# Kernel optimization log

Measured on AMD Instinct MI355X. Metric: run time of the kernel, lower is better.

## Reference

```python
import jax, jax.numpy as jnp
import numpy as np

NUM_CORRESPONDENCES = 256
M, N, D = 8192, 8192, 256


def setup_inputs() -> dict:
    key = jax.random.key(0)
    k1, k2 = jax.random.split(key)
    ref = jax.random.normal(k1, (M, D), dtype=jnp.float32)
    src = jax.random.normal(k2, (N, D), dtype=jnp.float32)
    # pairwise_distance(normalized=True) assumes unit-norm features
    ref = ref / jnp.linalg.norm(ref, axis=-1, keepdims=True)
    src = src / jnp.linalg.norm(src, axis=-1, keepdims=True)
    return {"ref_feats": ref, "src_feats": src}


def reference(ref_feats, src_feats):
    # squared pairwise distance for normalized feats: ||r||^2 + ||s||^2 - 2 r.s = 2 - 2 r.s
    dist = 2.0 - 2.0 * jnp.einsum('md,nd->mn', ref_feats, src_feats)  # [M, N]
    scores = jnp.exp(-dist)
    # dual normalization: row-normalized * col-normalized
    ref_scores = scores / jnp.sum(scores, axis=1, keepdims=True)
    src_scores = scores / jnp.sum(scores, axis=0, keepdims=True)
    scores = ref_scores * src_scores
    n_cols = scores.shape[1]
    flat = scores.reshape(-1)
    k = min(NUM_CORRESPONDENCES, flat.shape[0])
    corr_scores, corr_indices = jax.lax.top_k(flat, k)
    ref_corr_indices = corr_indices // n_cols
    src_corr_indices = corr_indices % n_cols
    # masks are None -> ref_indices/src_indices are identity arange, no remap needed
    return ref_corr_indices, src_corr_indices, corr_scores
```

## Files before the change

kernel.cpp:

```cpp
#include <hip/hip_runtime.h>

#define MD 8192
#define ND 8192
#define DD 256
#define KTOP 256
#define CAND_T0 0.26f
#define NCAP 4096
#define NPAD 4096

typedef unsigned int u32;
typedef unsigned short u16;
typedef unsigned long long u64;

#define OFF_R    0
#define OFF_CP   65536
#define OFF_CNT  589824
#define OFF_CAND 589952
#define OFF_KEYS 606336
#define OFF_A16  655360
#define OFF_B16  (OFF_A16 + 4194304)
#define WS_REQ   (OFF_B16 + 4194304)

using f16x8 = __attribute__((ext_vector_type(8))) _Float16;
using f32x4  = __attribute__((ext_vector_type(4))) float;

#define AS1 __attribute__((address_space(1)))
#define AS3 __attribute__((address_space(3)))

__device__ __forceinline__ u16 f2h(float x) {
  union { _Float16 h; u16 u; } v;
  v.h = (_Float16)x;
  return v.u;
}

__global__ void k_init(double* __restrict__ R, double* __restrict__ CP, int* __restrict__ cnt) {
  int stride = gridDim.x * blockDim.x;
  for (int i = blockIdx.x * blockDim.x + threadIdx.x; i < MD + 8 * ND; i += stride) {
    if (i < MD) R[i] = 0.0;
    else CP[i - MD] = 0.0;
  }
  if (blockIdx.x == 0 && threadIdx.x == 0) *cnt = 0;
}

__global__ __launch_bounds__(256) void k_prep2(
    const float* __restrict__ A, const float* __restrict__ B,
    u16* __restrict__ A16p, u16* __restrict__ B16p,
    double* __restrict__ R, double* __restrict__ CP, int* __restrict__ cnt) {
  const int gid = blockIdx.x * 256 + threadIdx.x;
  if (gid < MD) R[gid] = 0.0;
  if (gid < 8 * ND) CP[gid] = 0.0;
  if (gid == 0) *cnt = 0;

  {
    float4 v = ((const float4*)A)[gid];
    ushort4 h;
    h.x = f2h(v.x); h.y = f2h(v.y); h.z = f2h(v.z); h.w = f2h(v.w);
    ((ushort4*)A16p)[gid] = h;
  }
  {
    float4 v = ((const float4*)B)[gid];
    ushort4 h;
    h.x = f2h(v.x); h.y = f2h(v.y); h.z = f2h(v.z); h.w = f2h(v.w);
    ((ushort4*)B16p)[gid] = h;
  }
}

__global__ __launch_bounds__(512, 2) void k_gemm_mfma(
    const u16* __restrict__ A16, const u16* __restrict__ B16,
    double* __restrict__ R, double* __restrict__ CP,
    int* __restrict__ cnt, u32* __restrict__ cand, int ncap) {
  __shared__ u16 sA[2][256][32];
  __shared__ u16 sB[2][256][32];
  __shared__ float sRcomb[4][2][128];
  __shared__ double sCcomb[4][64];

  const int tid = threadIdx.x;
  const int lane = tid & 63;
  const int wid = tid >> 6;
  const int wrow = wid >> 2;
  const int wcol = wid & 3;

  const int g = blockIdx.x;
  const int xcd = g & 7;
  const int l = g >> 3;
  const int rowTile = xcd * 4 + (l & 3);
  const int colTile = l >> 2;
  const int rowBase = rowTile * 256;
  const int colBase = colTile * 256;
  double* Cmy = CP + (size_t)xcd * ND;

  const int quad = lane >> 4, lo = lane & 15;
  const int sw = (lo >> 1) & 3;
  const int cswz = (lane & 3) ^ ((lane >> 3) & 3);

  u16* lb0;
  const u16* gbl;
  if (wid < 4) {
    lb0 = &sA[0][wid * 64][0];
    gbl = A16 + (size_t)(rowBase + wid * 64 + (lane >> 2)) * DD + cswz * 8;
  } else {
    lb0 = &sB[0][(wid - 4) * 64][0];
    gbl = B16 + (size_t)(colBase + (wid - 4) * 64 + (lane >> 2)) * DD + cswz * 8;
  }

#define STAGE(b, kt) \
  do { \
    _Pragma("unroll") \
    for (int ch = 0; ch < 4; ++ch) { \
      const u16* gp = gbl + (size_t)(ch * 16) * DD + (kt) * 32; \
      __builtin_amdgcn_global_load_lds((const AS1 void*)gp, \
          (AS3 void*)(lb0 + (b) * 8192 + ch * 512), 16, 0, 0); \
    } \
  } while (0)

  f32x4 acc[8][4];
#pragma unroll
  for (int i = 0; i < 8; ++i)
#pragma unroll
    for (int j = 0; j < 4; ++j) acc[i][j] = (f32x4){0.f, 0.f, 0.f, 0.f};

  const int cq = (quad ^ sw) * 8;

  STAGE(0, 0);
  __syncthreads();

#pragma unroll
  for (int kt = 0; kt < 8; ++kt) {
    const int cur = kt & 1;
    if (kt < 7) STAGE(cur ^ 1, kt + 1);

    f16x8 fa[8];
#pragma unroll
    for (int t = 0; t < 8; ++t)
      fa[t] = *(const f16x8*)&sA[cur][wrow * 128 + t * 16 + lo][cq];
#pragma unroll
    for (int j = 0; j < 4; ++j) {
      f16x8 fb = *(const f16x8*)&sB[cur][wcol * 64 + j * 16 + lo][cq];
#pragma unroll
      for (int i = 0; i < 8; ++i)
        acc[i][j] = __builtin_amdgcn_mfma_f32_16x16x32_f16(fa[i], fb, acc[i][j], 0, 0, 0);
    }
    __syncthreads();
  }
#undef STAGE

  float rowp[8][4];
  double colp[4];
#pragma unroll
  for (int i = 0; i < 8; ++i)
#pragma unroll
    for (int r = 0; r < 4; ++r) rowp[i][r] = 0.f;
#pragma unroll
  for (int j = 0; j < 4; ++j) colp[j] = 0.0;

#pragma unroll
  for (int i = 0; i < 8; ++i)
#pragma unroll
    for (int j = 0; j < 4; ++j)
#pragma unroll
      for (int r = 0; r < 4; ++r) {
        float c = acc[i][j][r];
        float e = __expf(2.f * c - 2.f);
        rowp[i][r] += e;
        colp[j] += (double)e;
        if (c >= CAND_T0) {
          int row = rowBase + wrow * 128 + i * 16 + quad * 4 + r;
          int col = colBase + wcol * 64 + j * 16 + lo;
          int idx = atomicAdd(cnt, 1);
          if (idx < ncap) cand[idx] = ((u32)row << 13) | (u32)col;
        }
      }

#pragma unroll
  for (int i = 0; i < 8; ++i)
#pragma unroll
    for (int r = 0; r < 4; ++r) {
      float v = rowp[i][r];
#pragma unroll
      for (int off = 8; off; off >>= 1) v += __shfl_xor(v, off, 16);
      rowp[i][r] = v;
    }
#pragma unroll
  for (int j = 0; j < 4; ++j) {
    double v = colp[j];
    v += __shfl_xor(v, 16);
    v += __shfl_xor(v, 32);
    colp[j] = v;
  }

  if (wcol && lo == 0) {
#pragma unroll
    for (int i = 0; i < 8; ++i)
#pragma unroll
      for (int r = 0; r < 4; ++r)
        sRcomb[wcol][wrow][i * 16 + quad * 4 + r] = rowp[i][r];
  }
  if (wrow == 1 && quad == 0) {
#pragma unroll
    for (int j = 0; j < 4; ++j) sCcomb[wcol][j * 16 + lo] = colp[j];
  }
  __syncthreads();

  if (wcol == 0 && lo == 0) {
#pragma unroll
    for (int i = 0; i < 8; ++i)
#pragma unroll
      for (int r = 0; r < 4; ++r) {
        int idx = i * 16 + quad * 4 + r;
        float tot = rowp[i][r] + sRcomb[1][wrow][idx] + sRcomb[2][wrow][idx]
                  + sRcomb[3][wrow][idx];
        atomicAdd(&R[rowBase + wrow * 128 + idx], (double)tot);
      }
  }
  if (wrow == 0 && quad == 0) {
#pragma unroll
    for (int j = 0; j < 4; ++j) {
      int idx = j * 16 + lo;
      atomicAdd(&Cmy[colBase + wcol * 64 + idx], colp[j] + sCcomb[wcol][idx]);
    }
  }
}

__global__ __launch_bounds__(256) void k_gemm_f32(
    const float* __restrict__ A, const float* __restrict__ B,
    double* __restrict__ R, double* __restrict__ CP,
    int* __restrict__ cnt, u32* __restrict__ cand, int ncap) {
  __shared__ float As[32][128];
  __shared__ float Bs[32][128];
  __shared__ double colLds[16][128];
  const int tid = threadIdx.x;
  const int tx = tid & 15, ty = tid >> 4;
  const int rowBase = blockIdx.y * 128;
  const int colBase = blockIdx.x * 128;
  float acc[8][8];
#pragma unroll
  for (int i = 0; i < 8; ++i)
#pragma unroll
    for (int j = 0; j < 8; ++j) acc[i][j] = 0.f;
  const int lr = tid >> 3;
  const int lc = (tid & 7) << 2;
  for (int kk = 0; kk < DD; kk += 32) {
#pragma unroll
    for (int r = 0; r < 4; ++r) {
      int row = lr + r * 32;
      float4 av = *(const float4*)(A + (size_t)(rowBase + row) * DD + kk + lc);
      float4 bv = *(const float4*)(B + (size_t)(colBase + row) * DD + kk + lc);
      As[lc + 0][row] = av.x; As[lc + 1][row] = av.y; As[lc + 2][row] = av.z; As[lc + 3][row] = av.w;
      Bs[lc + 0][row] = bv.x; Bs[lc + 1][row] = bv.y; Bs[lc + 2][row] = bv.z; Bs[lc + 3][row] = bv.w;
    }
    __syncthreads();
#pragma unroll 4
    for (int k = 0; k < 32; ++k) {
      float a[8], b[8];
      *(float4*)(a + 0) = *(const float4*)(&As[k][ty * 8 + 0]);
      *(float4*)(a + 4) = *(const float4*)(&As[k][ty * 8 + 4]);
      *(float4*)(b + 0) = *(const float4*)(&Bs[k][tx * 8 + 0]);
      *(float4*)(b + 4) = *(const float4*)(&Bs[k][tx * 8 + 4]);
#pragma unroll
      for (int i = 0; i < 8; ++i)
#pragma unroll
        for (int j = 0; j < 8; ++j)
          acc[i][j] = fmaf(a[i], b[j], acc[i][j]);
    }
    __syncthreads();
  }
  double colpart[8];
#pragma unroll
  for (int j = 0; j < 8; ++j) colpart[j] = 0.0;
#pragma unroll
  for (int i = 0; i < 8; ++i) {
    double rp = 0.0;
#pragma unroll
    for (int j = 0; j < 8; ++j) {
      float e = __expf(2.f * acc[i][j] - 2.f);
      rp += (double)e;
      colpart[j] += (double)e;
    }
#pragma unroll
    for (int off = 8; off; off >>= 1) rp += __shfl_down(rp, off, 16);
    if (tx == 0) atomicAdd(&R[rowBase + ty * 8 + i], rp);
  }
#pragma unroll
  for (int j = 0; j < 8; ++j) colLds[ty][tx * 8 + j] = colpart[j];
  __syncthreads();
  if (tid < 128) {
    double s = 0.0;
#pragma unroll
    for (int t = 0; t < 16; ++t) s += colLds[t][tid];
    atomicAdd(&CP[colBase + tid], s);
  }
#pragma unroll
  for (int i = 0; i < 8; ++i)
#pragma unroll
    for (int j = 0; j < 8; ++j) {
      if (acc[i][j] >= CAND_T0) {
        int idx = atomicAdd(cnt, 1);
        if (idx < ncap)
          cand[idx] = ((u32)(rowBase + ty * 8 + i) << 13) | (u32)(colBase + tx * 8 + j);
      }
    }
}

__global__ __launch_bounds__(256) void k_score(
    const float* __restrict__ A, const float* __restrict__ B,
    const double* __restrict__ R, const double* __restrict__ CP,
    const int* __restrict__ cnt, const u32* __restrict__ cand,
    u64* __restrict__ keys, int ncap) {
  int w = (int)((blockIdx.x * 256 + threadIdx.x) >> 6);
  int lane = threadIdx.x & 63;
  int n = *cnt; if (n > ncap) n = ncap;
  if (w >= n) return;
  u32 mn = cand[w];
  int m = (int)(mn >> 13), nn = (int)(mn & 8191u);
  const float* ar = A + (size_t)m * DD;
  const float* br = B + (size_t)nn * DD;
  double s = 0.0;
#pragma unroll
  for (int d = 0; d < DD; d += 64)
    s = fma((double)ar[d + lane], (double)br[d + lane], s);
#pragma unroll
  for (int off = 32; off; off >>= 1) s += __shfl_down(s, off);
  if (lane == 0) {
    double Cn = 0.0;
#pragma unroll
    for (int x = 0; x < 8; ++x) Cn += CP[(size_t)x * ND + nn];
    double sc = exp(4.0 * s - 4.0) / (R[m] * Cn);
    keys[w] = (u64)__double_as_longlong(sc);
  }
}

__device__ __forceinline__ bool is_worse(u64 ka, u32 ma, u64 kb, u32 mb) {
  return (ka < kb) || (ka == kb && ma > mb);
}

__global__ __launch_bounds__(1024) void k_sort(
    const int* __restrict__ cnt, const u32* __restrict__ cand,
    const u64* __restrict__ keys, float* __restrict__ out, int ncap) {
  __shared__ u64 sk[NPAD];
  __shared__ u32 sm[NPAD];
  const int tid = threadIdx.x;
  const int lane = tid & 63;
  const int wid = tid >> 6;
  int m = *cnt; if (m > ncap) m = ncap;

  if (m <= 2048) {
    const int NP = (m <= 1024) ? 1024 : 2048;
    const int base = wid * 128;
    const int i0 = base + lane * 2;

    u64 k0 = (i0 < m) ? keys[i0] : 0;
    u64 k1 = (i0 + 1 < m) ? keys[i0 + 1] : 0;
    u32 m0 = (i0 < m) ? cand[i0] : 0xFFFFFFFFu;
    u32 m1 = (i0 + 1 < m) ? cand[i0 + 1] : 0xFFFFFFFFu;
#pragma unroll
    for (int k = 2; k <= 128; k <<= 1) {
#pragma unroll
      for (int j = k >> 1; j >= 1; j >>= 1) {
        const bool bf = ((i0 & k) == 0);
        if (j == 1) {
          bool sw = bf ? is_worse(k0, m0, k1, m1) : is_worse(k1, m1, k0, m0);
          if (sw) { u64 tk = k0; k0 = k1; k1 = tk; u32 tm = m0; m0 = m1; m1 = tm; }
        } else {
          const int j2 = j >> 1;
          const bool keepb = (bf == ((lane & j2) == 0));
          u64 pk0 = __shfl_xor(k0, j2); u32 pm0 = __shfl_xor(m0, j2);
          u64 pk1 = __shfl_xor(k1, j2); u32 pm1 = __shfl_xor(m1, j2);
          if (keepb == is_worse(k0, m0, pk0, pm0)) { k0 = pk0; m0 = pm0; }
          if (keepb == is_worse(k1, m1, pk1, pm1)) { k1 = pk1; m1 = pm1; }
        }
      }
    }
    sk[i0] = k0; sk[i0 + 1] = k1; sm[i0] = m0; sm[i0 + 1] = m1;
    __syncthreads();

    for (int k = 256; k <= NP; k <<= 1) {
      for (int j = k >> 1; j >= 128; j >>= 1) {
        for (int i = tid; i < NP; i += 1024) {
          int l = i ^ j;
          if (l > i) {
            u64 ki = sk[i], kl = sk[l];
            u32 mi = sm[i], ml = sm[l];
            bool bf = ((i & k) == 0);
            bool swp = bf ? is_worse(ki, mi, kl, ml) : is_worse(kl, ml, ki, mi);
            if (swp) { sk[i] = kl; sk[l] = ki; sm[i] = ml; sm[l] = mi; }
          }
        }
        __syncthreads();
      }
      if (i0 < NP) {
        k0 = sk[i0]; k1 = sk[i0 + 1]; m0 = sm[i0]; m1 = sm[i0 + 1];
        const bool bf = ((base & k) == 0);
#pragma unroll
        for (int j = 64; j >= 2; j >>= 1) {
          const int j2 = j >> 1;
          const bool keepb = (bf == ((lane & j2) == 0));
          u64 pk0 = __shfl_xor(k0, j2); u32 pm0 = __shfl_xor(m0, j2);
          u64 pk1 = __shfl_xor(k1, j2); u32 pm1 = __shfl_xor(m1, j2);
          if (keepb == is_worse(k0, m0, pk0, pm0)) { k0 = pk0; m0 = pm0; }
          if (keepb == is_worse(k1, m1, pk1, pm1)) { k1 = pk1; m1 = pm1; }
        }
        {
          bool sw = bf ? is_worse(k0, m0, k1, m1) : is_worse(k1, m1, k0, m0);
          if (sw) { u64 tk = k0; k0 = k1; k1 = tk; u32 tm = m0; m0 = m1; m1 = tm; }
        }
      }
      __syncthreads();
      if (i0 < NP) { sk[i0] = k0; sk[i0 + 1] = k1; sm[i0] = m0; sm[i0 + 1] = m1; }
      __syncthreads();
    }
  } else {
    for (int i = tid; i < NPAD; i += 1024) { sk[i] = 0; sm[i] = 0xFFFFFFFFu; }
    __syncthreads();
    for (int i = tid; i < m; i += 1024) { sk[i] = keys[i]; sm[i] = cand[i]; }
    __syncthreads();
    for (unsigned k = 2; k <= (unsigned)NPAD; k <<= 1) {
      for (unsigned j = k >> 1; j > 0; j >>= 1) {
        for (unsigned i = tid; i < (unsigned)NPAD; i += 1024) {
          unsigned l = i ^ j;
          if (l > i) {
            u64 ki = sk[i], kl = sk[l];
            u32 mi = sm[i], ml = sm[l];
            bool dir = ((i & k) == 0);
            bool swp = dir ? is_worse(ki, mi, kl, ml) : is_worse(kl, ml, ki, mi);
            if (swp) { sk[i] = kl; sk[l] = ki; sm[i] = ml; sm[l] = mi; }
          }
        }
        __syncthreads();
      }
    }
  }

  for (int r = tid; r < KTOP; r += 1024) {
    u32 mn = sm[r];
    u64 kk = sk[r];
    out[r] = (float)(mn >> 13);
    out[KTOP + r] = (float)(mn & 8191u);
    out[2 * KTOP + r] = (float)__longlong_as_double((long long)kk);
  }
}

extern "C" void kernel_launch(void* const* d_in, const int* in_sizes, int n_in,
                              void* d_out, int out_size, void* d_ws, size_t ws_size,
                              hipStream_t stream) {
  (void)in_sizes; (void)n_in; (void)out_size;
  const float* A = (const float*)d_in[0];
  const float* B = (const float*)d_in[1];
  float* out = (float*)d_out;
  char* ws = (char*)d_ws;
  double* R = (double*)(ws + OFF_R);
  double* CP = (double*)(ws + OFF_CP);
  int* cnt = (int*)(ws + OFF_CNT);
  u32* cand = (u32*)(ws + OFF_CAND);
  u64* keys = (u64*)(ws + OFF_KEYS);

  if (ws_size >= (size_t)WS_REQ) {
    u16* A16p = (u16*)(ws + OFF_A16);
    u16* B16p = (u16*)(ws + OFF_B16);
    hipLaunchKernelGGL(k_prep2, dim3(2048), dim3(256), 0, stream,
                       A, B, A16p, B16p, R, CP, cnt);
    hipLaunchKernelGGL(k_gemm_mfma, dim3(1024), dim3(512), 0, stream,
                       A16p, B16p, R, CP, cnt, cand, NCAP);
  } else {
    hipLaunchKernelGGL(k_init, dim3(288), dim3(256), 0, stream, R, CP, cnt);
    hipLaunchKernelGGL(k_gemm_f32, dim3(ND / 128, MD / 128), dim3(256), 0, stream,
                       A, B, R, CP, cnt, cand, NCAP);
  }

  hipLaunchKernelGGL(k_score, dim3(NCAP / 4), dim3(256), 0, stream,
                     A, B, R, CP, cnt, cand, keys, NCAP);
  hipLaunchKernelGGL(k_sort, dim3(1), dim3(1024), 0, stream,
                     cnt, cand, keys, out, NCAP);
}
```

Before: 151.2 us.

## Widen GEMM K-tile to 64 and interleave staged loads with MFMA phases

The K tile of the fused GEMM kernel doubles from 32 to 64, so the loop runs 4 iterations instead of 8, and the shared-memory swizzle changes to an XOR over rows mod 8. Each iteration is split into four quarter phases. In each phase fragment reads and part of the next tile's global-to-LDS loads are issued, then s_barrier and s_setprio wrap a block of MFMAs, aiming to overlap memory traffic with compute in a ping-pong style. The cost is double the LDS footprint for the staging buffers, which may hurt occupancy at 2 blocks per CU, plus extra barriers per iteration.

```diff
diff --git a/kernel.cpp b/kernel.cpp
--- a/kernel.cpp
+++ b/kernel.cpp
@@ -69,8 +69,8 @@
     const u16* __restrict__ A16, const u16* __restrict__ B16,
     double* __restrict__ R, double* __restrict__ CP,
     int* __restrict__ cnt, u32* __restrict__ cand, int ncap) {
-  __shared__ u16 sA[2][256][32];
-  __shared__ u16 sB[2][256][32];
+  __shared__ u16 sA[2][256][64];
+  __shared__ u16 sB[2][256][64];
   __shared__ float sRcomb[4][2][128];
   __shared__ double sCcomb[4][64];
 
@@ -90,28 +90,24 @@
   double* Cmy = CP + (size_t)xcd * ND;
 
   const int quad = lane >> 4, lo = lane & 15;
-  const int sw = (lo >> 1) & 3;
-  const int cswz = (lane & 3) ^ ((lane >> 3) & 3);
-
-  u16* lb0;
-  const u16* gbl;
-  if (wid < 4) {
-    lb0 = &sA[0][wid * 64][0];
-    gbl = A16 + (size_t)(rowBase + wid * 64 + (lane >> 2)) * DD + cswz * 8;
-  } else {
-    lb0 = &sB[0][(wid - 4) * 64][0];
-    gbl = B16 + (size_t)(colBase + (wid - 4) * 64 + (lane >> 2)) * DD + cswz * 8;
-  }
-
-#define STAGE(b, kt) \
-  do { \
-    _Pragma("unroll") \
-    for (int ch = 0; ch < 4; ++ch) { \
-      const u16* gp = gbl + (size_t)(ch * 16) * DD + (kt) * 32; \
-      __builtin_amdgcn_global_load_lds((const AS1 void*)gp, \
-          (AS3 void*)(lb0 + (b) * 8192 + ch * 512), 16, 0, 0); \
-    } \
-  } while (0)
+
+  const int srow = wid * 8 + (lane >> 3);
+  const int scol = ((lane & 7) ^ (lane >> 3)) * 8;
+  const u16* gA = A16 + (size_t)(rowBase + srow) * DD + scol;
+  const u16* gB = B16 + (size_t)(colBase + srow) * DD + scol;
+
+#define STAGE_A(nb, ktn, q) \
+  __builtin_amdgcn_global_load_lds( \
+      (const AS1 void*)(gA + (size_t)((q) * 64) * DD + (ktn) * 64), \
+      (AS3 void*)(&sA[nb][0][0] + (q) * 4096 + wid * 512), 16, 0, 0)
+#define STAGE_B(nb, ktn, q) \
+  __builtin_amdgcn_global_load_lds( \
+      (const AS1 void*)(gB + (size_t)((q) * 64) * DD + (ktn) * 64), \
+      (AS3 void*)(&sB[nb][0][0] + (q) * 4096 + wid * 512), 16, 0, 0)
+
+#define LDFRAG(buf, row, ks) \
+  (*(const f16x8*)&(buf)[(size_t)(row) * 64 + \
+      ((((ks) * 32 + quad * 8)) ^ (((row) & 7) * 8))])
 
   f32x4 acc[8][4];
 #pragma unroll
@@ -119,30 +115,95 @@
 #pragma unroll
     for (int j = 0; j < 4; ++j) acc[i][j] = (f32x4){0.f, 0.f, 0.f, 0.f};
 
-  const int cq = (quad ^ sw) * 8;
-
-  STAGE(0, 0);
+#pragma unroll
+  for (int q = 0; q < 4; ++q) { STAGE_A(0, 0, q); STAGE_B(0, 0, q); }
   __syncthreads();
 
 #pragma unroll
-  for (int kt = 0; kt < 8; ++kt) {
+  for (int kt = 0; kt < 4; ++kt) {
     const int cur = kt & 1;
-    if (kt < 7) STAGE(cur ^ 1, kt + 1);
-
-    f16x8 fa[8];
-#pragma unroll
-    for (int t = 0; t < 8; ++t)
-      fa[t] = *(const f16x8*)&sA[cur][wrow * 128 + t * 16 + lo][cq];
-#pragma unroll
-    for (int j = 0; j < 4; ++j) {
-      f16x8 fb = *(const f16x8*)&sB[cur][wcol * 64 + j * 16 + lo][cq];
-#pragma unroll
-      for (int i = 0; i < 8; ++i)
-        acc[i][j] = __builtin_amdgcn_mfma_f32_16x16x32_f16(fa[i], fb, acc[i][j], 0, 0, 0);
-    }
+    const int nb = cur ^ 1;
+    const u16* a0 = &sA[cur][0][0];
+    const u16* b0 = &sB[cur][0][0];
+    f16x8 fa[8][2], fb[4][2];
+
+#pragma unroll
+    for (int m = 0; m < 4; ++m)
+#pragma unroll
+      for (int ks = 0; ks < 2; ++ks)
+        fa[m][ks] = LDFRAG(a0, wrow * 128 + m * 16 + lo, ks);
+#pragma unroll
+    for (int n = 0; n < 2; ++n)
+#pragma unroll
+      for (int ks = 0; ks < 2; ++ks)
+        fb[n][ks] = LDFRAG(b0, wcol * 64 + n * 16 + lo, ks);
+    if (kt < 3) { STAGE_A(nb, kt + 1, 0); STAGE_A(nb, kt + 1, 1); }
+    __builtin_amdgcn_s_barrier();
+    __builtin_amdgcn_s_setprio(1);
+#pragma unroll
+    for (int ks = 0; ks < 2; ++ks)
+#pragma unroll
+      for (int n = 0; n < 2; ++n)
+#pragma unroll
+        for (int m = 0; m < 4; ++m)
+          acc[m][n] = __builtin_amdgcn_mfma_f32_16x16x32_f16(fa[m][ks], fb[n][ks], acc[m][n], 0, 0, 0);
+    __builtin_amdgcn_s_setprio(0);
+    __builtin_amdgcn_s_barrier();
+
+#pragma unroll
+    for (int m = 4; m < 8; ++m)
+#pragma unroll
+      for (int ks = 0; ks < 2; ++ks)
+        fa[m][ks] = LDFRAG(a0, wrow * 128 + m * 16 + lo, ks);
+    if (kt < 3) { STAGE_A(nb, kt + 1, 2); STAGE_A(nb, kt + 1, 3); }
+    __builtin_amdgcn_s_barrier();
+    __builtin_amdgcn_s_setprio(1);
+#pragma unroll
+    for (int ks = 0; ks < 2; ++ks)
+#pragma unroll
+      for (int n = 0; n < 2; ++n)
+#pragma unroll
+        for (int m = 4; m < 8; ++m)
+          acc[m][n] = __builtin_amdgcn_mfma_f32_16x16x32_f16(fa[m][ks], fb[n][ks], acc[m][n], 0, 0, 0);
+    __builtin_amdgcn_s_setprio(0);
+    __builtin_amdgcn_s_barrier();
+
+#pragma unroll
+    for (int n = 2; n < 4; ++n)
+#pragma unroll
+      for (int ks = 0; ks < 2; ++ks)
+        fb[n][ks] = LDFRAG(b0, wcol * 64 + n * 16 + lo, ks);
+    if (kt < 3) { STAGE_B(nb, kt + 1, 0); STAGE_B(nb, kt + 1, 1); }
+    __builtin_amdgcn_s_barrier();
+    __builtin_amdgcn_s_setprio(1);
+#pragma unroll
+    for (int ks = 0; ks < 2; ++ks)
+#pragma unroll
+      for (int n = 2; n < 4; ++n)
+#pragma unroll
+        for (int m = 0; m < 4; ++m)
+          acc[m][n] = __builtin_amdgcn_mfma_f32_16x16x32_f16(fa[m][ks], fb[n][ks], acc[m][n], 0, 0, 0);
+    __builtin_amdgcn_s_setprio(0);
+    __builtin_amdgcn_s_barrier();
+
+    if (kt < 3) { STAGE_B(nb, kt + 1, 2); STAGE_B(nb, kt + 1, 3); }
+    __builtin_amdgcn_s_barrier();
+    __builtin_amdgcn_s_setprio(1);
+#pragma unroll
+    for (int ks = 0; ks < 2; ++ks)
+#pragma unroll
+      for (int n = 2; n < 4; ++n)
+#pragma unroll
+        for (int m = 4; m < 8; ++m)
+          acc[m][n] = __builtin_amdgcn_mfma_f32_16x16x32_f16(fa[m][ks], fb[n][ks], acc[m][n], 0, 0, 0);
+    __builtin_amdgcn_s_setprio(0);
+
+    if (kt < 3) asm volatile("s_waitcnt vmcnt(0)" ::: "memory");
     __syncthreads();
   }
-#undef STAGE
+#undef STAGE_A
+#undef STAGE_B
+#undef LDFRAG
 
   float rowp[8][4];
   double colp[4];
```

New measurement: 150.5 us. No clear change (-0.5%).

## Restructure GEMM main loop into 64-wide K tiles with interleaved staged pipeline

Applied to the files above, without the earlier changes.

The MFMA GEMM main loop now uses 64-element K tiles instead of 32, so it runs 4 K-steps over two double buffers. Global-to-LDS loads for the next tiles are split into quarter chunks and interleaved between quadrant MFMA blocks, with explicit barriers, vmcnt/lgkmcnt waits, sched barriers and priority hints. LDS uses an XOR swizzle on rows of 64 halves. The goal is better overlap of memory with MFMA and fewer barriers per FLOP. In exchange LDS use per block doubles, register pressure rises, and the manual wait counts are fragile.

```diff
diff --git a/kernel.cpp b/kernel.cpp
--- a/kernel.cpp
+++ b/kernel.cpp
@@ -69,8 +69,8 @@
     const u16* __restrict__ A16, const u16* __restrict__ B16,
     double* __restrict__ R, double* __restrict__ CP,
     int* __restrict__ cnt, u32* __restrict__ cand, int ncap) {
-  __shared__ u16 sA[2][256][32];
-  __shared__ u16 sB[2][256][32];
+  __shared__ u16 sA[2][256][64];
+  __shared__ u16 sB[2][256][64];
   __shared__ float sRcomb[4][2][128];
   __shared__ double sCcomb[4][64];
 
@@ -90,59 +90,114 @@
   double* Cmy = CP + (size_t)xcd * ND;
 
   const int quad = lane >> 4, lo = lane & 15;
-  const int sw = (lo >> 1) & 3;
-  const int cswz = (lane & 3) ^ ((lane >> 3) & 3);
-
-  u16* lb0;
-  const u16* gbl;
-  if (wid < 4) {
-    lb0 = &sA[0][wid * 64][0];
-    gbl = A16 + (size_t)(rowBase + wid * 64 + (lane >> 2)) * DD + cswz * 8;
-  } else {
-    lb0 = &sB[0][(wid - 4) * 64][0];
-    gbl = B16 + (size_t)(colBase + (wid - 4) * 64 + (lane >> 2)) * DD + cswz * 8;
-  }
-
-#define STAGE(b, kt) \
-  do { \
-    _Pragma("unroll") \
-    for (int ch = 0; ch < 4; ++ch) { \
-      const u16* gp = gbl + (size_t)(ch * 16) * DD + (kt) * 32; \
-      __builtin_amdgcn_global_load_lds((const AS1 void*)gp, \
-          (AS3 void*)(lb0 + (b) * 8192 + ch * 512), 16, 0, 0); \
-    } \
-  } while (0)
+
+  const int srow = tid >> 3;
+  const int scol = ((tid & 7) ^ (srow & 7)) * 8;
+  const u16* gA = A16 + (size_t)(rowBase + srow) * DD + scol;
+  const u16* gB = B16 + (size_t)(colBase + srow) * DD + scol;
+  const int ldsseg = wid * 512;
+
+#define STG(M, b, ktn, H, r) \
+  __builtin_amdgcn_global_load_lds( \
+      (const AS1 void*)(g##M + (size_t)((H) * 128 + (r) * 64) * DD + (ktn) * 64), \
+      (AS3 void*)((u16*)&s##M[b][0][0] + (H) * 8192 + (r) * 4096 + ldsseg), 16, 0, 0)
+#define STGH(M, b, ktn, H) do { STG(M, b, ktn, H, 0); STG(M, b, ktn, H, 1); } while (0)
+
+#define LDF(M, b, row, ks) \
+  (*(const f16x8*)((const u16*)&s##M[b][0][0] + (size_t)(row) * 64 + \
+      (((ks) * 32 + quad * 8) ^ (((row) & 7) * 8))))
+
+#define RDA(b, m0) { _Pragma("unroll") \
+  for (int m = (m0); m < (m0) + 4; ++m) { _Pragma("unroll") \
+    for (int ks = 0; ks < 2; ++ks) fa[m][ks] = LDF(A, b, wrow * 128 + m * 16 + lo, ks); } }
+#define RDB(b, n0) { _Pragma("unroll") \
+  for (int n = (n0); n < (n0) + 2; ++n) { _Pragma("unroll") \
+    for (int ks = 0; ks < 2; ++ks) fb[n][ks] = LDF(B, b, wcol * 64 + n * 16 + lo, ks); } }
+#define MM(m0, n0) { _Pragma("unroll") \
+  for (int ks = 0; ks < 2; ++ks) { _Pragma("unroll") \
+    for (int n = (n0); n < (n0) + 2; ++n) { _Pragma("unroll") \
+      for (int m = (m0); m < (m0) + 4; ++m) \
+        acc[m][n] = __builtin_amdgcn_mfma_f32_16x16x32_f16(fa[m][ks], fb[n][ks], acc[m][n], 0, 0, 0); } } }
+
+#define SBAR  __builtin_amdgcn_s_barrier()
+#define SCHB  __builtin_amdgcn_sched_barrier(0)
+#define LGKM0 asm volatile("s_waitcnt lgkmcnt(0)" ::: "memory")
+#define VMC(n) asm volatile("s_waitcnt vmcnt(" #n ")" ::: "memory")
+#define PRIO1 __builtin_amdgcn_s_setprio(1)
+#define PRIO0 __builtin_amdgcn_s_setprio(0)
 
   f32x4 acc[8][4];
 #pragma unroll
   for (int i = 0; i < 8; ++i)
 #pragma unroll
     for (int j = 0; j < 4; ++j) acc[i][j] = (f32x4){0.f, 0.f, 0.f, 0.f};
-
-  const int cq = (quad ^ sw) * 8;
-
-  STAGE(0, 0);
-  __syncthreads();
-
-#pragma unroll
-  for (int kt = 0; kt < 8; ++kt) {
-    const int cur = kt & 1;
-    if (kt < 7) STAGE(cur ^ 1, kt + 1);
-
-    f16x8 fa[8];
-#pragma unroll
-    for (int t = 0; t < 8; ++t)
-      fa[t] = *(const f16x8*)&sA[cur][wrow * 128 + t * 16 + lo][cq];
-#pragma unroll
-    for (int j = 0; j < 4; ++j) {
-      f16x8 fb = *(const f16x8*)&sB[cur][wcol * 64 + j * 16 + lo][cq];
-#pragma unroll
-      for (int i = 0; i < 8; ++i)
-        acc[i][j] = __builtin_amdgcn_mfma_f32_16x16x32_f16(fa[i], fb, acc[i][j], 0, 0, 0);
-    }
-    __syncthreads();
-  }
-#undef STAGE
+  f16x8 fa[8][2], fb[4][2];
+
+  STGH(A, 0, 0, 0); STGH(A, 0, 0, 1); STGH(B, 0, 0, 0); STGH(B, 0, 0, 1);
+  STGH(A, 1, 1, 0); STGH(A, 1, 1, 1); STGH(B, 1, 1, 0); STGH(B, 1, 1, 1);
+  VMC(8);
+  SBAR;
+
+#pragma unroll
+  for (int it = 0; it < 2; ++it) {
+    const int k0 = 2 * it;
+    const bool more = (it < 1);
+
+    SCHB;
+    RDA(0, 0); RDB(0, 0);
+    if (it > 0) STGH(B, 1, k0 + 1, 0);
+    SBAR; LGKM0;
+    PRIO1; MM(0, 0); PRIO0;
+    SBAR;
+    SCHB;
+    RDA(0, 4);
+    if (it > 0) STGH(B, 1, k0 + 1, 1);
+    SBAR; LGKM0;
+    PRIO1; MM(4, 0); PRIO0;
+    SBAR;
+    SCHB;
+    RDB(0, 2);
+    if (more) STGH(A, 0, k0 + 2, 0);
+    SBAR; LGKM0;
+    PRIO1; MM(0, 2); PRIO0;
+    SBAR;
+    SCHB;
+    if (more) STGH(A, 0, k0 + 2, 1);
+    SBAR;
+    PRIO1; MM(4, 2); PRIO0;
+    if (more) { VMC(4); } else { VMC(0); }
+    SBAR;
+    SCHB;
+    RDA(1, 0); RDB(1, 0);
+    if (more) STGH(B, 0, k0 + 2, 0);
+    SBAR; LGKM0;
+    PRIO1; MM(0, 0); PRIO0;
+    SBAR;
+    SCHB;
+    RDA(1, 4);
+    if (more) STGH(B, 0, k0 + 2, 1);
+    SBAR; LGKM0;
+    PRIO1; MM(4, 0); PRIO0;
+    SBAR;
+    SCHB;
+    RDB(1, 2);
+    if (more) STGH(A, 1, k0 + 3, 0);
+    SBAR; LGKM0;
+    PRIO1; MM(0, 2); PRIO0;
+    SBAR;
+    SCHB;
+    if (more) STGH(A, 1, k0 + 3, 1);
+    SBAR;
+    PRIO1; MM(4, 2); PRIO0;
+    if (more) VMC(4);
+    SBAR;
+  }
+#undef STG
+#undef STGH
+#undef LDF
+#undef RDA
+#undef RDB
+#undef MM
 
   float rowp[8][4];
   double colp[4];
```

Result: no change. 149.4 us (-1.1%).
